# Kernel optimization log

Hardware: AMD Instinct MI355X
Metric: run time of the kernel (lower is better)

The kernel has to match this reference:

```python
import jax, jax.numpy as jnp
import numpy as np

RES_UP_RATIO = 0.05   # reserve_up_ratio (mgr.args default)
RES_DN_RATIO = 0.02   # reserve_dn_ratio
REQ_UP_RATIO = 0.02   # system_reserve_up_ratio
REQ_DN_RATIO = 0.02   # system_reserve_dn_ratio


def _build_K(G):
    """Static constraint matrix of the per-timestep LP over x=[P, R_up, R_dn] (n=3G).
    Row 0 is the equality sum(P)=D; remaining rows are <= inequalities."""
    n = 3 * G
    m = 1 + 4 * G + 2
    K = np.zeros((m, n), dtype=np.float32)
    I = np.eye(G, dtype=np.float32)
    K[0, :G] = 1.0                      # sum_g P = D
    r = 1
    K[r:r+G, :G] = I;  K[r:r+G, G:2*G] = I;  r += G      # P + R_up <= pmax
    K[r:r+G, :G] = -I; K[r:r+G, 2*G:3*G] = I; r += G     # -P + R_dn <= -pmin
    K[r:r+G, :G] = I;  r += G                             # P <= pmax
    K[r:r+G, :G] = -I; r += G                             # -P <= -pmin
    K[r, G:2*G] = -1.0; r += 1                            # -sum R_up <= -req_up*D
    K[r, 2*G:3*G] = -1.0                                  # -sum R_dn <= -req_dn*D
    return K


def _solve_da_lp(forecast, pmin, pmax, b, n_iters):
    """Batched PDHG (Chambolle-Pock) solve of all B*T per-timestep LPs.
    Returns P, R_up, R_dn with shape (B, T, G)."""
    B, T = forecast.shape
    G = b.shape[0]
    Knp = _build_K(G)
    L = float(np.linalg.norm(Knp, 2))          # static spectral norm of K
    tau = sigma = 0.9 / L
    K = jnp.asarray(Knp)
    m, n = K.shape
    # objective coefficients over x=[P, R_up, R_dn] (Cost = b*P + c is affine)
    c_obj = jnp.concatenate([b, RES_UP_RATIO * b, RES_DN_RATIO * b])  # (n,)
    # rhs q: (B, T, m)
    q = jnp.concatenate([
        forecast[..., None],
        jnp.broadcast_to(pmax, (B, T, G)),
        jnp.broadcast_to(-pmin, (B, T, G)),
        jnp.broadcast_to(pmax, (B, T, G)),
        jnp.broadcast_to(-pmin, (B, T, G)),
        -REQ_UP_RATIO * forecast[..., None],
        -REQ_DN_RATIO * forecast[..., None],
    ], axis=-1)
    ineq = (jnp.arange(m) > 0)  # row 0 = equality dual (unprojected)

    x0 = jnp.zeros((B, T, n), dtype=forecast.dtype)
    y0 = jnp.zeros((B, T, m), dtype=forecast.dtype)

    def step(carry, _):
        x, y = carry
        x_new = jnp.maximum(x - tau * (c_obj + jnp.einsum('btm,mn->btn', y, K)), 0.0)
        x_bar = 2.0 * x_new - x
        y_new = y + sigma * (jnp.einsum('btn,mn->btm', x_bar, K) - q)
        y_new = jnp.where(ineq, jnp.maximum(y_new, 0.0), y_new)
        return (x_new, y_new), None

    (x, _), _ = jax.lax.scan(step, (x0, y0), None, length=n_iters)
    P = x[..., :G]
    Ru = x[..., G:2*G]
    Rd = x[..., 2*G:3*G]
    return P, Ru, Rd


def setup_inputs() -> dict:
    key = jax.random.key(0)
    k1, k2, k3, k4 = jax.random.split(key, 4)
    G, B, T = 50, 128, 24
    pmax = 100.0 + 400.0 * jax.random.uniform(k1, (G,), dtype=jnp.float32)
    pmin = 0.1 * pmax
    b = 20.0 + 30.0 * jax.random.uniform(k2, (G,), dtype=jnp.float32)
    c = 100.0 * jax.random.uniform(k3, (G,), dtype=jnp.float32)
    lo, hi = jnp.sum(pmin), jnp.sum(pmax)
    # feasible demand: comfortably inside [sum pmin, sum pmax] so reserves exist
    forecast = lo + (0.35 + 0.3 * jax.random.uniform(k4, (B, T), dtype=jnp.float32)) * (hi - lo)
    return {"forecast": forecast, "pmin": pmin, "pmax": pmax, "b": b, "c": c, "n_iters": 300}


def reference(forecast, pmin, pmax, b, c, n_iters):
    P, Ru, Rd = _solve_da_lp(forecast, pmin, pmax, b, n_iters)  # (B,T,G)
    # match torch layout (B, G, T)
    P_DA = jnp.swapaxes(P, 1, 2)
    R_up = jnp.swapaxes(Ru, 1, 2)
    R_dn = jnp.swapaxes(Rd, 1, 2)
    Cost_DA = b[None, :, None] * P_DA + c[None, :, None]
    ru_price = (RES_UP_RATIO * b)[None, :, None]
    rd_price = (RES_DN_RATIO * b)[None, :, None]
    obj = Cost_DA.sum((1, 2)) + (ru_price * R_up).sum((1, 2)) + (rd_price * R_dn).sum((1, 2))
    return (P_DA, R_up, R_dn, obj, Cost_DA)
```

## Files before the change

### kernel.cpp

```cpp
#include <hip/hip_runtime.h>
#include <math.h>

#define G   50
#define T   24
#define B   128
#define NLP (B * T)
#define SZ  (B * G * T)

typedef float v2f __attribute__((ext_vector_type(2)));


__device__ __forceinline__ v2f vmax0(v2f v) {
    v2f z = {0.f, 0.f};
    return __builtin_elementwise_max(v, z);
}

template <int CTRL>
__device__ __forceinline__ float dpp_mov(float x) {
    int r = __builtin_amdgcn_update_dpp(0, __float_as_int(x), CTRL, 0xf, 0xf, true);
    return __int_as_float(r);
}

__device__ __forceinline__ float swz_xor16(float x) {
    return __int_as_float(__builtin_amdgcn_ds_swizzle(__float_as_int(x), 0x401F));
}

__device__ __forceinline__ void half_sum3(float& a, float& b, float& c) {
    a += dpp_mov<0x121>(a); b += dpp_mov<0x121>(b); c += dpp_mov<0x121>(c);
    a += dpp_mov<0x122>(a); b += dpp_mov<0x122>(b); c += dpp_mov<0x122>(c);
    a += dpp_mov<0x124>(a); b += dpp_mov<0x124>(b); c += dpp_mov<0x124>(c);
    a += dpp_mov<0x128>(a); b += dpp_mov<0x128>(b); c += dpp_mov<0x128>(c);
    a += swz_xor16(a);      b += swz_xor16(b);      c += swz_xor16(c);
}

__device__ __forceinline__ float half_sum1(float a) {
    a += dpp_mov<0x121>(a);
    a += dpp_mov<0x122>(a);
    a += dpp_mov<0x124>(a);
    a += dpp_mov<0x128>(a);
    a += swz_xor16(a);
    return a;
}

__device__ __forceinline__ float wave_sum1(float a) {
    a += dpp_mov<0x121>(a);
    a += dpp_mov<0x122>(a);
    a += dpp_mov<0x124>(a);
    a += dpp_mov<0x128>(a);
    a += swz_xor16(a);
    float lo = __int_as_float(__builtin_amdgcn_readlane(__float_as_int(a), 0));
    float hi = __int_as_float(__builtin_amdgcn_readlane(__float_as_int(a), 32));
    return lo + hi;
}

__global__ __launch_bounds__(64)
void pdhg_lp_kernel(const float* __restrict__ forecast,
                    const float* __restrict__ pmin,
                    const float* __restrict__ pmax,
                    const float* __restrict__ bcost,
                    const float* __restrict__ ccost,
                    const int*   __restrict__ n_iters_p,
                    float* __restrict__ out,
                    float* __restrict__ ws_partial,
                    float tau)
{
    const int lane = threadIdx.x;
    const int lh   = lane & 31;
    const int half = lane >> 5;
    const int lp   = blockIdx.x * 2 + half;
    const int b    = lp / T;
    const int t    = lp - b * T;
    const int n_iters = n_iters_p[0];

    const int  g0 = lh;
    const int  g1 = lh + 32;
    const bool a1 = (g1 < G);

    v2f bj  = { bcost[g0], a1 ? bcost[g1] : 0.f };
    v2f cj  = { ccost[g0], a1 ? ccost[g1] : 0.f };
    v2f pmx = { pmax[g0],  a1 ? pmax[g1]  : 0.f };
    v2f pmn = { pmin[g0],  a1 ? pmin[g1]  : 0.f };
    const float f = forecast[lp];

    const float ts  = tau * tau;
    const float BIG = 1e30f;

    v2f tcP  = tau * bj;          if (!a1) tcP.y  = BIG;
    v2f tcRu = (tau * 0.05f) * bj; if (!a1) tcRu.y = BIG;
    v2f tcRd = (tau * 0.02f) * bj; if (!a1) tcRd.y = BIG;
    v2f tspmx = ts * pmx;
    v2f tspmn = ts * pmn;
    const float tsf   = ts * f;
    const float tsreq = ts * 0.02f * f;

    v2f P = {0,0}, Ru = {0,0}, Rd = {0,0};
    v2f z1 = {0,0}, z2 = {0,0}, z3 = {0,0}, z4 = {0,0};
    float z0 = 0.f, zru = 0.f, zrd = 0.f;

    for (int it = 0; it < n_iters; ++it) {
        v2f gP = (z1 - z2) + (z3 - z4) + z0;
        v2f Pn = vmax0(P - tcP - gP);
        v2f Run = vmax0(Ru - tcRu - (z1 - zru));
        v2f Rdn = vmax0(Rd - tcRd - (z2 - zrd));

        v2f Pb  = 2.f * Pn  - P;
        v2f Rub = 2.f * Run - Ru;
        v2f Rdb = 2.f * Rdn - Rd;
        P = Pn; Ru = Run; Rd = Rdn;

        float sP  = Pb.x  + Pb.y;
        float sRu = Rub.x + Rub.y;
        float sRd = Rdb.x + Rdb.y;
        half_sum3(sP, sRu, sRd);

        z0  = z0 + ts * sP - tsf;
        z1  = vmax0(z1 + ts * (Pb + Rub) - tspmx);
        z2  = vmax0(z2 + ts * (Rdb - Pb) + tspmn);
        z3  = vmax0(z3 + ts * Pb - tspmx);
        z4  = vmax0(z4 - ts * Pb + tspmn);
        zru = fmaxf(zru + tsreq - ts * sRu, 0.f);
        zrd = fmaxf(zrd + tsreq - ts * sRd, 0.f);
    }

    const v2f cost = bj * P + cj;
    {
        const int base0 = b * (G * T) + g0 * T + t;
        out[base0]              = P.x;
        out[SZ + base0]         = Ru.x;
        out[2 * SZ + base0]     = Rd.x;
        out[3 * SZ + B + base0] = cost.x;
        if (a1) {
            const int base1 = b * (G * T) + g1 * T + t;
            out[base1]              = P.y;
            out[SZ + base1]         = Ru.y;
            out[2 * SZ + base1]     = Rd.y;
            out[3 * SZ + B + base1] = cost.y;
        }
    }

    if (ws_partial) {
        v2f lo2 = cost + (0.05f * bj) * Ru + (0.02f * bj) * Rd;
        float tot = half_sum1(lo2.x + lo2.y);
        if (lh == 0) ws_partial[lp] = tot;
    }
}

__global__ __launch_bounds__(64)
void obj_final_kernel(const float* __restrict__ ws_partial, float* __restrict__ out)
{
    const int b = blockIdx.x * 64 + threadIdx.x;
    if (b < B) {
        float s = 0.f;
        #pragma unroll
        for (int t = 0; t < T; ++t) s += ws_partial[b * T + t];
        out[3 * SZ + b] = s;
    }
}

__global__ __launch_bounds__(256)
void obj_kernel(const float* __restrict__ bcost, float* __restrict__ out)
{
    const int b = blockIdx.x;
    const float* Ru = out + SZ     + (size_t)b * (G * T);
    const float* Rd = out + 2 * SZ + (size_t)b * (G * T);
    const float* C  = out + 3 * SZ + B + (size_t)b * (G * T);

    float s = 0.f;
    for (int i = threadIdx.x; i < G * T; i += 256) {
        const int g = i / T;
        const float bg = bcost[g];
        s += C[i] + 0.05f * bg * Ru[i] + 0.02f * bg * Rd[i];
    }
    __shared__ float sm[4];
    s = wave_sum1(s);
    if ((threadIdx.x & 63) == 0) sm[threadIdx.x >> 6] = s;
    __syncthreads();
    if (threadIdx.x == 0) out[3 * SZ + b] = (sm[0] + sm[1]) + (sm[2] + sm[3]);
}

extern "C" void kernel_launch(void* const* d_in, const int* in_sizes, int n_in,
                              void* d_out, int out_size, void* d_ws, size_t ws_size,
                              hipStream_t stream) {
    const float* forecast = (const float*)d_in[0];
    const float* pmin_p   = (const float*)d_in[1];
    const float* pmax_p   = (const float*)d_in[2];
    const float* b_p      = (const float*)d_in[3];
    const float* c_p      = (const float*)d_in[4];
    const int*   niter_p  = (const int*)  d_in[5];
    float* out = (float*)d_out;

    const double L = sqrt((105.0 + sqrt(17.0)) * 0.5);
    const float tau = (float)(0.9 / L);

    const bool use_ws = (ws_size >= (size_t)NLP * sizeof(float));
    float* wsp = use_ws ? (float*)d_ws : nullptr;

    pdhg_lp_kernel<<<NLP / 2, 64, 0, stream>>>(forecast, pmin_p, pmax_p,
                                               b_p, c_p, niter_p, out, wsp, tau);
    if (use_ws) {
        obj_final_kernel<<<(B + 63) / 64, 64, 0, stream>>>(wsp, out);
    } else {
        obj_kernel<<<B, 256, 0, stream>>>(b_p, out);
    }
}
```

Measured before the change: 147.2 us.

## Pack four LPs per wave with 16-lane rows and four generators per lane

Each 64-lane wave now solves four per-timestep LPs instead of two: every 16-lane DPP row handles one LP, and each lane holds four generators in two v2f groups. The cross-lane sum no longer needs the ds_swizzle xor-16 step and uses only row-local DPP adds, which removes an LDS-path instruction from the serial dependency chain of every iteration. It also halves the number of wavefronts and raises per-lane ALU work and register use. With fewer waves there is less latency hiding on the GPU. The fallback objective kernel is adjusted to reduce with row sums over 16 shared slots.

Result: faster. 137.9 us (-6.3%).

```diff
diff --git a/kernel.cpp b/kernel.cpp
--- a/kernel.cpp
+++ b/kernel.cpp
@@ -21,36 +21,19 @@
     return __int_as_float(r);
 }
 
-__device__ __forceinline__ float swz_xor16(float x) {
-    return __int_as_float(__builtin_amdgcn_ds_swizzle(__float_as_int(x), 0x401F));
-}
-
-__device__ __forceinline__ void half_sum3(float& a, float& b, float& c) {
+__device__ __forceinline__ void row_sum3(float& a, float& b, float& c) {
     a += dpp_mov<0x121>(a); b += dpp_mov<0x121>(b); c += dpp_mov<0x121>(c);
     a += dpp_mov<0x122>(a); b += dpp_mov<0x122>(b); c += dpp_mov<0x122>(c);
     a += dpp_mov<0x124>(a); b += dpp_mov<0x124>(b); c += dpp_mov<0x124>(c);
     a += dpp_mov<0x128>(a); b += dpp_mov<0x128>(b); c += dpp_mov<0x128>(c);
-    a += swz_xor16(a);      b += swz_xor16(b);      c += swz_xor16(c);
-}
-
-__device__ __forceinline__ float half_sum1(float a) {
+}
+
+__device__ __forceinline__ float row_sum1(float a) {
     a += dpp_mov<0x121>(a);
     a += dpp_mov<0x122>(a);
     a += dpp_mov<0x124>(a);
     a += dpp_mov<0x128>(a);
-    a += swz_xor16(a);
     return a;
-}
-
-__device__ __forceinline__ float wave_sum1(float a) {
-    a += dpp_mov<0x121>(a);
-    a += dpp_mov<0x122>(a);
-    a += dpp_mov<0x124>(a);
-    a += dpp_mov<0x128>(a);
-    a += swz_xor16(a);
-    float lo = __int_as_float(__builtin_amdgcn_readlane(__float_as_int(a), 0));
-    float hi = __int_as_float(__builtin_amdgcn_readlane(__float_as_int(a), 32));
-    return lo + hi;
 }
 
 __global__ __launch_bounds__(64)
@@ -65,82 +48,102 @@
                     float tau)
 {
     const int lane = threadIdx.x;
-    const int lh   = lane & 31;
-    const int half = lane >> 5;
-    const int lp   = blockIdx.x * 2 + half;
+    const int lh   = lane & 15;
+    const int row  = lane >> 4;
+    const int lp   = blockIdx.x * 4 + row;
     const int b    = lp / T;
     const int t    = lp - b * T;
     const int n_iters = n_iters_p[0];
 
-    const int  g0 = lh;
-    const int  g1 = lh + 32;
-    const bool a1 = (g1 < G);
-
-    v2f bj  = { bcost[g0], a1 ? bcost[g1] : 0.f };
-    v2f cj  = { ccost[g0], a1 ? ccost[g1] : 0.f };
-    v2f pmx = { pmax[g0],  a1 ? pmax[g1]  : 0.f };
-    v2f pmn = { pmin[g0],  a1 ? pmin[g1]  : 0.f };
+    const int  gA0 = lh,      gA1 = lh + 16;
+    const int  gB0 = lh + 32;
+    const int  gB1 = lh + 48;
+    const bool vB1 = (lh < 2);
+
+    v2f bjA  = { bcost[gA0], bcost[gA1] };
+    v2f bjB  = { bcost[gB0], vB1 ? bcost[gB1] : 0.f };
+    v2f cjA  = { ccost[gA0], ccost[gA1] };
+    v2f cjB  = { ccost[gB0], vB1 ? ccost[gB1] : 0.f };
+    v2f pmxA = { pmax[gA0],  pmax[gA1] };
+    v2f pmxB = { pmax[gB0],  vB1 ? pmax[gB1] : 0.f };
+    v2f pmnA = { pmin[gA0],  pmin[gA1] };
+    v2f pmnB = { pmin[gB0],  vB1 ? pmin[gB1] : 0.f };
     const float f = forecast[lp];
 
     const float ts  = tau * tau;
     const float BIG = 1e30f;
 
-    v2f tcP  = tau * bj;          if (!a1) tcP.y  = BIG;
-    v2f tcRu = (tau * 0.05f) * bj; if (!a1) tcRu.y = BIG;
-    v2f tcRd = (tau * 0.02f) * bj; if (!a1) tcRd.y = BIG;
-    v2f tspmx = ts * pmx;
-    v2f tspmn = ts * pmn;
+    v2f tcPA  = tau * bjA;
+    v2f tcPB  = tau * bjB;           if (!vB1) tcPB.y  = BIG;
+    v2f tcRuA = (tau * 0.05f) * bjA;
+    v2f tcRuB = (tau * 0.05f) * bjB; if (!vB1) tcRuB.y = BIG;
+    v2f tcRdA = (tau * 0.02f) * bjA;
+    v2f tcRdB = (tau * 0.02f) * bjB; if (!vB1) tcRdB.y = BIG;
+    v2f tspmxA = ts * pmxA, tspmxB = ts * pmxB;
+    v2f tspmnA = ts * pmnA, tspmnB = ts * pmnB;
     const float tsf   = ts * f;
     const float tsreq = ts * 0.02f * f;
 
-    v2f P = {0,0}, Ru = {0,0}, Rd = {0,0};
-    v2f z1 = {0,0}, z2 = {0,0}, z3 = {0,0}, z4 = {0,0};
+    v2f PA = {0,0}, PB = {0,0}, RuA = {0,0}, RuB = {0,0}, RdA = {0,0}, RdB = {0,0};
+    v2f z1A = {0,0}, z1B = {0,0}, z2A = {0,0}, z2B = {0,0};
+    v2f z3A = {0,0}, z3B = {0,0}, z4A = {0,0}, z4B = {0,0};
     float z0 = 0.f, zru = 0.f, zrd = 0.f;
 
     for (int it = 0; it < n_iters; ++it) {
-        v2f gP = (z1 - z2) + (z3 - z4) + z0;
-        v2f Pn = vmax0(P - tcP - gP);
-        v2f Run = vmax0(Ru - tcRu - (z1 - zru));
-        v2f Rdn = vmax0(Rd - tcRd - (z2 - zrd));
-
-        v2f Pb  = 2.f * Pn  - P;
-        v2f Rub = 2.f * Run - Ru;
-        v2f Rdb = 2.f * Rdn - Rd;
-        P = Pn; Ru = Run; Rd = Rdn;
-
-        float sP  = Pb.x  + Pb.y;
-        float sRu = Rub.x + Rub.y;
-        float sRd = Rdb.x + Rdb.y;
-        half_sum3(sP, sRu, sRd);
+        v2f z0v = { z0, z0 };
+        v2f zruv = { zru, zru };
+        v2f zrdv = { zrd, zrd };
+        v2f gPA = (z1A - z2A) + (z3A - z4A) + z0v;
+        v2f gPB = (z1B - z2B) + (z3B - z4B) + z0v;
+        v2f PnA = vmax0(PA - tcPA - gPA);
+        v2f PnB = vmax0(PB - tcPB - gPB);
+        v2f RunA = vmax0(RuA - tcRuA - z1A + zruv);
+        v2f RunB = vmax0(RuB - tcRuB - z1B + zruv);
+        v2f RdnA = vmax0(RdA - tcRdA - z2A + zrdv);
+        v2f RdnB = vmax0(RdB - tcRdB - z2B + zrdv);
+
+        v2f PbA  = 2.f * PnA  - PA,  PbB  = 2.f * PnB  - PB;
+        v2f RubA = 2.f * RunA - RuA, RubB = 2.f * RunB - RuB;
+        v2f RdbA = 2.f * RdnA - RdA, RdbB = 2.f * RdnB - RdB;
+        PA = PnA; PB = PnB; RuA = RunA; RuB = RunB; RdA = RdnA; RdB = RdnB;
+
+        v2f tP = PbA + PbB, tRu = RubA + RubB, tRd = RdbA + RdbB;
+        float sP  = tP.x  + tP.y;
+        float sRu = tRu.x + tRu.y;
+        float sRd = tRd.x + tRd.y;
+        row_sum3(sP, sRu, sRd);
 
         z0  = z0 + ts * sP - tsf;
-        z1  = vmax0(z1 + ts * (Pb + Rub) - tspmx);
-        z2  = vmax0(z2 + ts * (Rdb - Pb) + tspmn);
-        z3  = vmax0(z3 + ts * Pb - tspmx);
-        z4  = vmax0(z4 - ts * Pb + tspmn);
+        z1A = vmax0(z1A + ts * (PbA + RubA) - tspmxA);
+        z1B = vmax0(z1B + ts * (PbB + RubB) - tspmxB);
+        z2A = vmax0(z2A + ts * (RdbA - PbA) + tspmnA);
+        z2B = vmax0(z2B + ts * (RdbB - PbB) + tspmnB);
+        z3A = vmax0(z3A + ts * PbA - tspmxA);
+        z3B = vmax0(z3B + ts * PbB - tspmxB);
+        z4A = vmax0(z4A - ts * PbA + tspmnA);
+        z4B = vmax0(z4B - ts * PbB + tspmnB);
         zru = fmaxf(zru + tsreq - ts * sRu, 0.f);
         zrd = fmaxf(zrd + tsreq - ts * sRd, 0.f);
     }
 
-    const v2f cost = bj * P + cj;
+    const v2f costA = bjA * PA + cjA;
+    const v2f costB = bjB * PB + cjB;
     {
-        const int base0 = b * (G * T) + g0 * T + t;
-        out[base0]              = P.x;
-        out[SZ + base0]         = Ru.x;
-        out[2 * SZ + base0]     = Rd.x;
-        out[3 * SZ + B + base0] = cost.x;
-        if (a1) {
-            const int base1 = b * (G * T) + g1 * T + t;
-            out[base1]              = P.y;
-            out[SZ + base1]         = Ru.y;
-            out[2 * SZ + base1]     = Rd.y;
-            out[3 * SZ + B + base1] = cost.y;
+        const int bgt = b * (G * T) + t;
+        const int a0 = bgt + gA0 * T, a1 = bgt + gA1 * T, b0 = bgt + gB0 * T;
+        out[a0] = PA.x;  out[SZ + a0] = RuA.x;  out[2*SZ + a0] = RdA.x;  out[3*SZ + B + a0] = costA.x;
+        out[a1] = PA.y;  out[SZ + a1] = RuA.y;  out[2*SZ + a1] = RdA.y;  out[3*SZ + B + a1] = costA.y;
+        out[b0] = PB.x;  out[SZ + b0] = RuB.x;  out[2*SZ + b0] = RdB.x;  out[3*SZ + B + b0] = costB.x;
+        if (vB1) {
+            const int b1 = bgt + gB1 * T;
+            out[b1] = PB.y;  out[SZ + b1] = RuB.y;  out[2*SZ + b1] = RdB.y;  out[3*SZ + B + b1] = costB.y;
         }
     }
 
     if (ws_partial) {
-        v2f lo2 = cost + (0.05f * bj) * Ru + (0.02f * bj) * Rd;
-        float tot = half_sum1(lo2.x + lo2.y);
+        v2f lo = costA + (0.05f * bjA) * RuA + (0.02f * bjA) * RdA
+               + costB + (0.05f * bjB) * RuB + (0.02f * bjB) * RdB;
+        float tot = row_sum1(lo.x + lo.y);
         if (lh == 0) ws_partial[lp] = tot;
     }
 }
@@ -171,11 +174,16 @@
         const float bg = bcost[g];
         s += C[i] + 0.05f * bg * Ru[i] + 0.02f * bg * Rd[i];
     }
-    __shared__ float sm[4];
-    s = wave_sum1(s);
-    if ((threadIdx.x & 63) == 0) sm[threadIdx.x >> 6] = s;
+    __shared__ float sm[16];
+    s = row_sum1(s);
+    if ((threadIdx.x & 15) == 0) sm[threadIdx.x >> 4] = s;
     __syncthreads();
-    if (threadIdx.x == 0) out[3 * SZ + b] = (sm[0] + sm[1]) + (sm[2] + sm[3]);
+    if (threadIdx.x == 0) {
+        float tot = 0.f;
+        #pragma unroll
+        for (int i = 0; i < 16; ++i) tot += sm[i];
+        out[3 * SZ + b] = tot;
+    }
 }
 
 extern "C" void kernel_launch(void* const* d_in, const int* in_sizes, int n_in,
@@ -195,7 +203,7 @@
     const bool use_ws = (ws_size >= (size_t)NLP * sizeof(float));
     float* wsp = use_ws ? (float*)d_ws : nullptr;
 
-    pdhg_lp_kernel<<<NLP / 2, 64, 0, stream>>>(forecast, pmin_p, pmax_p,
+    pdhg_lp_kernel<<<NLP / 4, 64, 0, stream>>>(forecast, pmin_p, pmax_p,
                                                b_p, c_p, niter_p, out, wsp, tau);
     if (use_ws) {
         obj_final_kernel<<<(B + 63) / 64, 64, 0, stream>>>(wsp, out);
```
